# Kernel tuning notes

Measured on AMD Instinct MI355X. Metric: run time of the kernel, lower is better.

The kernel has to match this reference:

```python
import jax, jax.numpy as jnp
import numpy as np

N, HIDDEN, HEADS, HEAD = 20000, 128, 8, 16
LAP, NBUCKETS, NBINS, MAXDEG, E = 16, 1024, 32, 64, 320000


def _mlp(x, W1, b1, W2, b2):
    return jax.nn.relu(x @ W1 + b1) @ W2 + b2


def _build_pairs(bq, bk, edge_index):
    """Host-side: P_LSH = {(i,j)!=: bq[i]==bk[j]} union graph edges, deduped.
    Mirrors _lsh_pairs + torch.unique (data-dependent size -> numpy)."""
    bq = np.asarray(bq); bk = np.asarray(bk); ei = np.asarray(edge_index)
    srcs = [ei[0].astype(np.int64)]; dsts = [ei[1].astype(np.int64)]
    common = np.intersect1d(np.unique(bq), np.unique(bk))
    for b in common:
        qn = np.nonzero(bq == b)[0]
        kn = np.nonzero(bk == b)[0]
        ii = np.repeat(qn, kn.size)
        jj = np.tile(kn, qn.size)
        m = ii != jj
        srcs.append(ii[m].astype(np.int64)); dsts.append(jj[m].astype(np.int64))
    src = np.concatenate(srcs); dst = np.concatenate(dsts)
    code = np.unique(src * np.int64(N) + dst)  # dedup pairs
    return jnp.asarray(code // N, jnp.int32), jnp.asarray(code % N, jnp.int32)


def setup_inputs() -> dict:
    key = jax.random.key(0)
    ks = jax.random.split(key, 16)
    rn = lambda k, sh, s=1.0: (jax.random.normal(k, sh, jnp.float32) * s)
    d_in = HIDDEN + LAP
    return {
        "Q": rn(ks[0], (N, HIDDEN)),
        "K": rn(ks[1], (N, HIDDEN)),
        "V": rn(ks[2], (N, HIDDEN)),
        "lap_pe": jax.random.uniform(ks[3], (N, LAP), jnp.float32),
        "W_q1": rn(ks[4], (d_in, HIDDEN), d_in ** -0.5), "b_q1": jnp.zeros((HIDDEN,), jnp.float32),
        "W_q2": rn(ks[5], (HIDDEN, NBUCKETS), HIDDEN ** -0.5), "b_q2": jnp.zeros((NBUCKETS,), jnp.float32),
        "W_k1": rn(ks[6], (d_in, HIDDEN), d_in ** -0.5), "b_k1": jnp.zeros((HIDDEN,), jnp.float32),
        "W_k2": rn(ks[7], (HIDDEN, NBUCKETS), HIDDEN ** -0.5), "b_k2": jnp.zeros((NBUCKETS,), jnp.float32),
        "spd_bias": rn(ks[8], (NBINS + 1, HEADS), 0.02),
        "deg_src_emb": rn(ks[9], (MAXDEG + 2, HEADS), 0.02),
        "deg_dst_emb": rn(ks[10], (MAXDEG + 2, HEADS), 0.02),
        "W_out": rn(ks[11], (HIDDEN, HIDDEN), HIDDEN ** -0.5), "b_out": jnp.zeros((HIDDEN,), jnp.float32),
        "spd_boundaries": jnp.linspace(0.0, 2.0, NBINS).astype(jnp.float32),
        "edge_index": jax.random.randint(ks[12], (2, E), 0, N, jnp.int32),
        "deg": jax.random.randint(ks[13], (N,), 0, MAXDEG + 1, jnp.int32),
    }


def reference(Q, K, V, lap_pe, W_q1, b_q1, W_q2, b_q2, W_k1, b_k1, W_k2, b_k2,
              spd_bias, deg_src_emb, deg_dst_emb, W_out, b_out, spd_boundaries,
              edge_index, deg):
    q_in = jnp.concatenate([Q, lap_pe], axis=-1)
    k_in = jnp.concatenate([K, lap_pe], axis=-1)
    l_q = _mlp(q_in, W_q1, b_q1, W_q2, b_q2)  # (N, B)
    l_k = _mlp(k_in, W_k1, b_k1, W_k2, b_k2)
    src, dst = _build_pairs(jnp.argmax(l_q, -1), jnp.argmax(l_k, -1), edge_index)

    Qh = Q.reshape(N, HEADS, HEAD)
    Kh = K.reshape(N, HEADS, HEAD)
    Vh = V.reshape(N, HEADS, HEAD)

    scores = jnp.einsum("ehd,ehd->eh", Qh[src], Kh[dst]) / (HEAD ** 0.5)  # (P, H)
    pe_dist = jnp.linalg.norm(lap_pe[src] - lap_pe[dst], axis=-1)
    spd_idx = jnp.searchsorted(spd_boundaries, pe_dist, side="left")  # torch.bucketize(right=False)
    scores = scores + spd_bias[spd_idx]
    dsrc = jnp.clip(deg[src], 0, MAXDEG + 1)
    ddst = jnp.clip(deg[dst], 0, MAXDEG + 1)
    scores = scores + deg_src_emb[dsrc] + deg_dst_emb[ddst]

    # pyg_softmax: segment softmax over src index
    m = jax.ops.segment_max(scores, src, num_segments=N)  # (N, H)
    m = jnp.where(jnp.isneginf(m), 0.0, m)
    ex = jnp.exp(scores - m[src])
    denom = jax.ops.segment_sum(ex, src, num_segments=N)
    alpha = ex / (denom[src] + 1e-16)  # dropout p=0 (eval)

    h = jax.ops.segment_sum(alpha[..., None] * Vh[dst], src, num_segments=N)
    h_global = h.reshape(N, HIDDEN) @ W_out + b_out
    return h_global, l_q, l_k
```

## Files before the change

kernel.cpp:

```cpp
#include <hip/hip_runtime.h>
#include <math.h>

#define NN 20000
#define HID 128
#define NH 8
#define HD 16
#define LAPD 16
#define NB 1024
#define NBINS 32
#define MAXDEG 64
#define NE 320000
#define DIN 144

#define NEGH (-1.0e30f)

__global__ __launch_bounds__(256) void mlp_kernel(
    const float* __restrict__ X, const float* __restrict__ lap,
    const float* __restrict__ W1, const float* __restrict__ b1,
    const float* __restrict__ W2, const float* __restrict__ b2,
    float* __restrict__ outL, int* __restrict__ bidx)
{
    __shared__ __align__(16) float xs[16][DIN];
    __shared__ __align__(16) float hs[16][HID];
    __shared__ float rbv[64];
    __shared__ int   rbi[64];
    const int tid = threadIdx.x;
    const int n0 = blockIdx.x * 16;

    for (int e = tid; e < 16 * DIN; e += 256) {
        int n = e / DIN, k = e - n * DIN;
        float v = (k < HID) ? X[(size_t)(n0 + n) * HID + k]
                            : lap[(size_t)(n0 + n) * LAPD + (k - HID)];
        xs[n][k] = v;
    }
    __syncthreads();

    const int c = tid & 127, ng = tid >> 7;
    float hacc[8];
    {
        float bb = b1[c];
        #pragma unroll
        for (int m = 0; m < 8; m++) hacc[m] = bb;
        for (int k = 0; k < DIN; k += 4) {
            float w0 = W1[(k + 0) * HID + c];
            float w1 = W1[(k + 1) * HID + c];
            float w2 = W1[(k + 2) * HID + c];
            float w3 = W1[(k + 3) * HID + c];
            #pragma unroll
            for (int m = 0; m < 8; m++) {
                float4 xv = *(const float4*)&xs[ng * 8 + m][k];
                hacc[m] = fmaf(xv.x, w0, hacc[m]);
                hacc[m] = fmaf(xv.y, w1, hacc[m]);
                hacc[m] = fmaf(xv.z, w2, hacc[m]);
                hacc[m] = fmaf(xv.w, w3, hacc[m]);
            }
        }
    }
    #pragma unroll
    for (int m = 0; m < 8; m++) hs[ng * 8 + m][c] = fmaxf(hacc[m], 0.0f);
    __syncthreads();

    float a0[16], a1[16], a2[16], a3[16];
    #pragma unroll
    for (int m = 0; m < 16; m++) { a0[m] = 0.f; a1[m] = 0.f; a2[m] = 0.f; a3[m] = 0.f; }

    const float* W2b = W2 + 4 * tid;
    float4 w0 = *(const float4*)&W2b[(size_t)0 * NB];
    float4 w1 = *(const float4*)&W2b[(size_t)1 * NB];
    float4 w2 = *(const float4*)&W2b[(size_t)2 * NB];
    float4 w3 = *(const float4*)&W2b[(size_t)3 * NB];
    for (int k = 0; k < HID; k += 4) {
        const int kn = (k + 4 < HID) ? (k + 4) : 0;
        float4 nw0 = *(const float4*)&W2b[(size_t)(kn + 0) * NB];
        float4 nw1 = *(const float4*)&W2b[(size_t)(kn + 1) * NB];
        float4 nw2 = *(const float4*)&W2b[(size_t)(kn + 2) * NB];
        float4 nw3 = *(const float4*)&W2b[(size_t)(kn + 3) * NB];
        #pragma unroll
        for (int m = 0; m < 16; m++) {
            const float4 hv = *(const float4*)&hs[m][k];
            a0[m] = fmaf(hv.x, w0.x, fmaf(hv.y, w1.x, fmaf(hv.z, w2.x, fmaf(hv.w, w3.x, a0[m]))));
            a1[m] = fmaf(hv.x, w0.y, fmaf(hv.y, w1.y, fmaf(hv.z, w2.y, fmaf(hv.w, w3.y, a1[m]))));
            a2[m] = fmaf(hv.x, w0.z, fmaf(hv.y, w1.z, fmaf(hv.z, w2.z, fmaf(hv.w, w3.z, a2[m]))));
            a3[m] = fmaf(hv.x, w0.w, fmaf(hv.y, w1.w, fmaf(hv.z, w2.w, fmaf(hv.w, w3.w, a3[m]))));
        }
        w0 = nw0; w1 = nw1; w2 = nw2; w3 = nw3;
    }

    const float4 bb4 = *(const float4*)&b2[4 * tid];
    const int lane = tid & 63, wv = tid >> 6;
    const int o0 = 4 * tid;
    for (int m = 0; m < 16; m++) {
        float4 ov;
        ov.x = a0[m] + bb4.x; ov.y = a1[m] + bb4.y;
        ov.z = a2[m] + bb4.z; ov.w = a3[m] + bb4.w;
        *(float4*)&outL[(size_t)(n0 + m) * NB + o0] = ov;
        float bv = ov.x; int bi = o0;
        if (ov.y > bv) { bv = ov.y; bi = o0 + 1; }
        if (ov.z > bv) { bv = ov.z; bi = o0 + 2; }
        if (ov.w > bv) { bv = ov.w; bi = o0 + 3; }
        #pragma unroll
        for (int off = 1; off < 64; off <<= 1) {
            float ovv = __shfl_xor(bv, off, 64);
            int   oi  = __shfl_xor(bi, off, 64);
            if (ovv > bv || (ovv == bv && oi < bi)) { bv = ovv; bi = oi; }
        }
        if (lane == 0) { rbv[wv * 16 + m] = bv; rbi[wv * 16 + m] = bi; }
    }
    __syncthreads();
    if (tid < 16) {
        float bv = rbv[tid]; int bi = rbi[tid];
        #pragma unroll
        for (int ww = 1; ww < 4; ww++) {
            float ov = rbv[ww * 16 + tid]; int oi = rbi[ww * 16 + tid];
            if (ov > bv || (ov == bv && oi < bi)) { bv = ov; bi = oi; }
        }
        bidx[n0 + tid] = min(max(bi, 0), NB - 1);
    }
}

__global__ void zero_kernel(int* __restrict__ p, int n) {
    int i = blockIdx.x * 256 + threadIdx.x;
    if (i < n) p[i] = 0;
}

__global__ void hist_kernel(const int* __restrict__ bkarr, int* __restrict__ bcnt) {
    int i = blockIdx.x * 256 + threadIdx.x;
    if (i < NN) {
        int b = min(max(bkarr[i], 0), NB - 1);
        atomicAdd(&bcnt[b], 1);
    }
}

__global__ __launch_bounds__(1024) void scan_bucket_kernel(const int* __restrict__ cnt,
        int* __restrict__ off, int* __restrict__ fill) {
    __shared__ int s[1024];
    int t = threadIdx.x;
    int v = cnt[t];
    s[t] = v; __syncthreads();
    for (int o = 1; o < 1024; o <<= 1) {
        int a = (t >= o) ? s[t - o] : 0;
        __syncthreads();
        s[t] += a;
        __syncthreads();
    }
    int excl = s[t] - v;
    off[t] = excl; fill[t] = excl;
    if (t == 1023) off[NB] = s[1023];
}

__global__ __launch_bounds__(1024) void order_kernel(
    const int* __restrict__ boff,
    const int* __restrict__ qcnt,
    int* __restrict__ qfill)
{
    __shared__ int kk[1024];
    __shared__ int ii[1024];
    __shared__ int ss[1024];
    const int t = threadIdx.x;
    kk[t] = boff[t + 1] - boff[t];
    ii[t] = t;
    __syncthreads();
    for (int size = 2; size <= 1024; size <<= 1) {
        for (int stride = size >> 1; stride > 0; stride >>= 1) {
            const int p = t ^ stride;
            if (p > t) {
                const int k1 = kk[t], k2 = kk[p];
                const bool up = ((t & size) == 0);
                if ((k1 < k2) == up) {
                    const int i1 = ii[t];
                    kk[t] = k2; kk[p] = k1;
                    ii[t] = ii[p]; ii[p] = i1;
                }
            }
            __syncthreads();
        }
    }
    const int v = qcnt[ii[t]];
    ss[t] = v; __syncthreads();
    for (int o = 1; o < 1024; o <<= 1) {
        int a = (t >= o) ? ss[t - o] : 0;
        __syncthreads();
        ss[t] += a;
        __syncthreads();
    }
    qfill[ii[t]] = ss[t] - v;
}

__global__ void scatter_bucket_kernel(const int* __restrict__ bkarr,
        int* __restrict__ fill, int* __restrict__ blist) {
    int i = blockIdx.x * 256 + threadIdx.x;
    if (i < NN) {
        int b = min(max(bkarr[i], 0), NB - 1);
        int p = atomicAdd(&fill[b], 1);
        if (p >= 0 && p < NN) blist[p] = i;
    }
}

__global__ __launch_bounds__(1024) void scan_edge_kernel(const int* __restrict__ cnt,
        int* __restrict__ off, int* __restrict__ fill) {
    __shared__ int s[1024];
    const int t = threadIdx.x;
    const int base = t * 20;
    int loc[20]; int sum = 0;
    #pragma unroll
    for (int k = 0; k < 20; k++) {
        int idx = base + k;
        int v = (idx < NN) ? cnt[idx] : 0;
        loc[k] = sum; sum += v;
    }
    s[t] = sum; __syncthreads();
    for (int o = 1; o < 1024; o <<= 1) {
        int a = (t >= o) ? s[t - o] : 0;
        __syncthreads();
        s[t] += a;
        __syncthreads();
    }
    int pre = s[t] - sum;
    #pragma unroll
    for (int k = 0; k < 20; k++) {
        int idx = base + k;
        if (idx < NN) { int e = pre + loc[k]; off[idx] = e; fill[idx] = e; }
    }
    if (t == 1023) off[NN] = s[1023];
}

__global__ void edge_count_kernel(const int* __restrict__ ei, int* __restrict__ ecnt) {
    int e = blockIdx.x * 256 + threadIdx.x;
    if (e < NE) {
        int s = min(max(ei[e], 0), NN - 1);
        atomicAdd(&ecnt[s], 1);
    }
}

__global__ void edge_scatter_kernel(const int* __restrict__ ei,
        int* __restrict__ fill, int* __restrict__ adj) {
    int e = blockIdx.x * 256 + threadIdx.x;
    if (e < NE) {
        int s = min(max(ei[e], 0), NN - 1);
        int d = min(max(ei[NE + e], 0), NN - 1);
        int p = atomicAdd(&fill[s], 1);
        if (p >= 0 && p < NE) adj[p] = d;
    }
}

__global__ __launch_bounds__(256) void dedup_kernel(
    const int* __restrict__ eoff, int* __restrict__ adj,
    const int* __restrict__ bqv, const int* __restrict__ bkv,
    int* __restrict__ acnt)
{
    __shared__ int prev[4][192];
    const int lane = threadIdx.x & 63, wv = threadIdx.x >> 6;
    const int i = blockIdx.x * 4 + wv;
    if (i >= NN) return;
    int es = eoff[i], ee = eoff[i + 1];
    es = min(max(es, 0), NE); ee = min(max(ee, es), NE);
    const int d = ee - es;
    const int b = min(max(bqv[i], 0), NB - 1);
    int kept = 0;
    for (int t0 = 0; t0 < d; t0 += 64) {
        const int t = t0 + lane;
        const bool in = t < d;
        int j = -1;
        if (in) j = min(max(adj[es + t], 0), NN - 1);
        bool keep = in && ((j == i) || (bkv[j] != b));
        const int nin = min(64, d - t0);
        for (int q2 = 0; q2 < nin; q2++) {
            int jq = __shfl(j, q2, 64);
            if (in && q2 < lane && jq == j) keep = false;
        }
        if (t0 > 0 && in) {
            asm volatile("s_waitcnt lgkmcnt(0)" ::: "memory");
            const int np = min(t0, 192);
            for (int q2 = 0; q2 < np; q2++)
                if (prev[wv][q2] == j) keep = false;
        }
        if (in && t < 192) prev[wv][t] = j;
        unsigned long long km = __ballot(keep);
        int pos = __popcll(km & ((1ull << lane) - 1ull));
        if (keep) adj[es + kept + pos] = j;
        kept += (int)__popcll(km);
    }
    if (lane == 0) acnt[i] = kept;
}

__global__ __launch_bounds__(256) void attn_kernel(
    const float* __restrict__ Q, const float* __restrict__ K, const float* __restrict__ V,
    const float* __restrict__ lap,
    const float* __restrict__ spdb, const float* __restrict__ dse,
    const float* __restrict__ dde, const float* __restrict__ bndr,
    const int* __restrict__ deg,
    const int* __restrict__ bq,
    const int* __restrict__ boff, const int* __restrict__ blist,
    const int* __restrict__ eoff, const int* __restrict__ acnt,
    const int* __restrict__ adj, const int* __restrict__ qlist,
    float* __restrict__ outH)
{
    __shared__ __align__(16) float qfl[4][128];
    __shared__ __align__(16) float pefl[4][16];
    __shared__ float wts[4][8][66];
    __shared__ int   jls[4][64];
    __shared__ __align__(16) float spdbs[(NBINS + 1) * NH];
    __shared__ __align__(16) float ddes[(MAXDEG + 2) * NH];
    __shared__ float bnd[32];

    const int tid = threadIdx.x;
    const int wv = tid >> 6, lane = tid & 63;
    const int cq = lane >> 2, qq = lane & 3;

    const int task = (int)blockIdx.x * 4 + wv;
    int i = qlist[task];
    i = min(max(i, 0), NN - 1);

    for (int e = tid; e < (NBINS + 1) * NH; e += 256) spdbs[e] = spdb[e];
    for (int e = tid; e < (MAXDEG + 2) * NH; e += 256) ddes[e] = dde[e];
    if (tid < 32) bnd[tid] = bndr[tid];
    qfl[wv][lane]      = Q[(size_t)i * HID + lane];
    qfl[wv][lane + 64] = Q[(size_t)i * HID + 64 + lane];
    if (lane < 16) pefl[wv][lane] = lap[(size_t)i * LAPD + lane];

    int b = min(max(bq[i], 0), NB - 1);
    int bs = boff[b], be = boff[b + 1];
    bs = min(max(bs, 0), NN); be = min(max(be, bs), NN);
    int es = eoff[i];
    es = min(max(es, 0), NE);
    int na = min(max(acnt[i], 0), NE - es);
    const int Lb = be - bs;
    const int Ltot = Lb + na;
    const int degi = min(max(deg[i], 0), MAXDEG + 1);

    int jn = i; bool vn = false;
    if (lane < Ltot) {
        if (lane < Lb) {
            jn = min(max(blist[bs + lane], 0), NN - 1);
            vn = (jn != i);
        } else {
            jn = min(max(adj[es + (lane - Lb)], 0), NN - 1);
            vn = true;
        }
    }
    __syncthreads();

    const float4 ds0 = *(const float4*)&dse[degi * 8];
    const float4 ds1 = *(const float4*)&dse[degi * 8 + 4];

    float m8[8], l8[8];
    #pragma unroll
    for (int h = 0; h < 8; h++) { m8[h] = NEGH; l8[h] = 0.0f; }
    float acc[32];
    #pragma unroll
    for (int k = 0; k < 32; k++) acc[k] = 0.0f;

    for (int t0 = 0; t0 < Ltot; t0 += 64) {
        const int j = jn; const bool valid = vn;

        float s8[8];
        if (valid) {
            const float4* K4 = (const float4*)(K + (size_t)j * HID);
            const float4* Q4 = (const float4*)&qfl[wv][0];
            #pragma unroll
            for (int h = 0; h < 8; h++) {
                float4 k0 = K4[h * 4 + 0], k1 = K4[h * 4 + 1];
                float4 k2 = K4[h * 4 + 2], k3 = K4[h * 4 + 3];
                float4 q0 = Q4[h * 4 + 0], q1 = Q4[h * 4 + 1];
                float4 q2 = Q4[h * 4 + 2], q3 = Q4[h * 4 + 3];
                float dot = 0.0f;
                dot = fmaf(q0.x, k0.x, dot); dot = fmaf(q0.y, k0.y, dot);
                dot = fmaf(q0.z, k0.z, dot); dot = fmaf(q0.w, k0.w, dot);
                dot = fmaf(q1.x, k1.x, dot); dot = fmaf(q1.y, k1.y, dot);
                dot = fmaf(q1.z, k1.z, dot); dot = fmaf(q1.w, k1.w, dot);
                dot = fmaf(q2.x, k2.x, dot); dot = fmaf(q2.y, k2.y, dot);
                dot = fmaf(q2.z, k2.z, dot); dot = fmaf(q2.w, k2.w, dot);
                dot = fmaf(q3.x, k3.x, dot); dot = fmaf(q3.y, k3.y, dot);
                dot = fmaf(q3.z, k3.z, dot); dot = fmaf(q3.w, k3.w, dot);
                s8[h] = dot * 0.25f;
            }
            const float4* P4 = (const float4*)&pefl[wv][0];
            const float4* L4 = (const float4*)(lap + (size_t)j * LAPD);
            float ss = 0.0f;
            #pragma unroll
            for (int d4 = 0; d4 < 4; d4++) {
                float4 pe = P4[d4], lj = L4[d4];
                float dx = pe.x - lj.x, dy = pe.y - lj.y;
                float dz = pe.z - lj.z, dw = pe.w - lj.w;
                ss = fmaf(dx, dx, ss); ss = fmaf(dy, dy, ss);
                ss = fmaf(dz, dz, ss); ss = fmaf(dw, dw, ss);
            }
            float dist = sqrtf(ss);
            int si = 0;
            #pragma unroll
            for (int kb = 0; kb < 32; kb++) si += (bnd[kb] < dist) ? 1 : 0;
            const int dj = min(max(deg[j], 0), MAXDEG + 1);
            const float4 sb0 = *(const float4*)&spdbs[si * 8];
            const float4 sb1 = *(const float4*)&spdbs[si * 8 + 4];
            const float4 db0 = *(const float4*)&ddes[dj * 8];
            const float4 db1 = *(const float4*)&ddes[dj * 8 + 4];
            s8[0] += sb0.x + ds0.x + db0.x; s8[1] += sb0.y + ds0.y + db0.y;
            s8[2] += sb0.z + ds0.z + db0.z; s8[3] += sb0.w + ds0.w + db0.w;
            s8[4] += sb1.x + ds1.x + db1.x; s8[5] += sb1.y + ds1.y + db1.y;
            s8[6] += sb1.z + ds1.z + db1.z; s8[7] += sb1.w + ds1.w + db1.w;
        } else {
            #pragma unroll
            for (int h = 0; h < 8; h++) s8[h] = NEGH;
        }
        jls[wv][lane] = valid ? j : i;

        jn = i; vn = false;
        {
            const int t2 = t0 + 64 + lane;
            if (t2 < Ltot) {
                if (t2 < Lb) {
                    jn = min(max(blist[bs + t2], 0), NN - 1);
                    vn = (jn != i);
                } else {
                    jn = min(max(adj[es + (t2 - Lb)], 0), NN - 1);
                    vn = true;
                }
            }
        }

        float alpha8[8];
        #pragma unroll
        for (int h = 0; h < 8; h++) {
            float cm = s8[h];
            #pragma unroll
            for (int off = 1; off < 64; off <<= 1)
                cm = fmaxf(cm, __shfl_xor(cm, off, 64));
            const float mn = fmaxf(m8[h], cm);
            alpha8[h] = __expf(m8[h] - mn);
            const float p = valid ? __expf(s8[h] - mn) : 0.0f;
            l8[h] = l8[h] * alpha8[h] + p;
            m8[h] = mn;
            wts[wv][h][lane] = p;
        }

        float aq0, aq1;
        if (qq == 0)      { aq0 = alpha8[0]; aq1 = alpha8[1]; }
        else if (qq == 1) { aq0 = alpha8[2]; aq1 = alpha8[3]; }
        else if (qq == 2) { aq0 = alpha8[4]; aq1 = alpha8[5]; }
        else              { aq0 = alpha8[6]; aq1 = alpha8[7]; }

        #pragma unroll
        for (int k = 0; k < 16; k++) acc[k] *= aq0;
        #pragma unroll
        for (int k = 16; k < 32; k++) acc[k] *= aq1;

        asm volatile("s_waitcnt lgkmcnt(0)" ::: "memory");

        const int rem = Ltot - t0;
        const int npass = ((rem < 64 ? rem : 64) + 15) >> 4;
        for (int r = 0; r < npass; r++) {
            const int cc = r * 16 + cq;
            const int jc = jls[wv][cc];
            const float w0 = wts[wv][2 * qq][cc];
            const float w1 = wts[wv][2 * qq + 1][cc];
            const float4* V4 = (const float4*)(V + (size_t)jc * HID + qq * 32);
            #pragma unroll
            for (int s = 0; s < 4; s++) {
                const float4 v = V4[s];
                acc[s * 4 + 0] = fmaf(w0, v.x, acc[s * 4 + 0]);
                acc[s * 4 + 1] = fmaf(w0, v.y, acc[s * 4 + 1]);
                acc[s * 4 + 2] = fmaf(w0, v.z, acc[s * 4 + 2]);
                acc[s * 4 + 3] = fmaf(w0, v.w, acc[s * 4 + 3]);
            }
            #pragma unroll
            for (int s = 4; s < 8; s++) {
                const float4 v = V4[s];
                acc[s * 4 + 0] = fmaf(w1, v.x, acc[s * 4 + 0]);
                acc[s * 4 + 1] = fmaf(w1, v.y, acc[s * 4 + 1]);
                acc[s * 4 + 2] = fmaf(w1, v.z, acc[s * 4 + 2]);
                acc[s * 4 + 3] = fmaf(w1, v.w, acc[s * 4 + 3]);
            }
        }
    }

    #pragma unroll
    for (int h = 0; h < 8; h++) {
        float v = l8[h];
        #pragma unroll
        for (int off = 1; off < 64; off <<= 1) v += __shfl_xor(v, off, 64);
        l8[h] = v;
    }
    float lq0, lq1;
    if (qq == 0)      { lq0 = l8[0]; lq1 = l8[1]; }
    else if (qq == 1) { lq0 = l8[2]; lq1 = l8[3]; }
    else if (qq == 2) { lq0 = l8[4]; lq1 = l8[5]; }
    else              { lq0 = l8[6]; lq1 = l8[7]; }
    const float linv0 = 1.0f / (lq0 + 1e-16f);
    const float linv1 = 1.0f / (lq1 + 1e-16f);
    #pragma unroll
    for (int k = 0; k < 16; k++) acc[k] *= linv0;
    #pragma unroll
    for (int k = 16; k < 32; k++) acc[k] *= linv1;

    #pragma unroll
    for (int k = 0; k < 32; k++) {
        float v = acc[k];
        v += __shfl_xor(v, 4, 64);
        v += __shfl_xor(v, 8, 64);
        v += __shfl_xor(v, 16, 64);
        v += __shfl_xor(v, 32, 64);
        acc[k] = v;
    }
    if (cq == 0) {
        float4* orow = (float4*)(outH + (size_t)i * HID + qq * 32);
        #pragma unroll
        for (int s = 0; s < 8; s++)
            orow[s] = make_float4(acc[s * 4 + 0], acc[s * 4 + 1],
                                  acc[s * 4 + 2], acc[s * 4 + 3]);
    }
}

__global__ __launch_bounds__(256) void out_gemm_kernel(
    const float* __restrict__ Wout, const float* __restrict__ bout,
    float* __restrict__ outH)
{
    __shared__ __align__(16) float hsT[32][HID];
    const int tid = threadIdx.x;
    const int r0 = blockIdx.x * 32;

    for (int e = tid; e < 32 * 32; e += 256) {
        const int r = e >> 5, c4 = e & 31;
        ((float4*)&hsT[r][0])[c4] = ((const float4*)&outH[(size_t)(r0 + r) * HID])[c4];
    }
    __syncthreads();

    const int c = tid & 127;
    const int mg = tid >> 7;
    float acc[16];
    const float bb = bout[c];
    #pragma unroll
    for (int m = 0; m < 16; m++) acc[m] = bb;

    for (int k = 0; k < HID; k += 4) {
        const float w0 = Wout[(size_t)(k + 0) * HID + c];
        const float w1 = Wout[(size_t)(k + 1) * HID + c];
        const float w2 = Wout[(size_t)(k + 2) * HID + c];
        const float w3 = Wout[(size_t)(k + 3) * HID + c];
        #pragma unroll
        for (int m = 0; m < 16; m++) {
            const float4 hv = *(const float4*)&hsT[mg * 16 + m][k];
            acc[m] = fmaf(hv.x, w0, fmaf(hv.y, w1, fmaf(hv.z, w2, fmaf(hv.w, w3, acc[m]))));
        }
    }
    #pragma unroll
    for (int m = 0; m < 16; m++)
        outH[(size_t)(r0 + mg * 16 + m) * HID + c] = acc[m];
}

extern "C" void kernel_launch(void* const* d_in, const int* in_sizes, int n_in,
                              void* d_out, int out_size, void* d_ws, size_t ws_size,
                              hipStream_t stream) {
    const float* Q    = (const float*)d_in[0];
    const float* Kx   = (const float*)d_in[1];
    const float* Vx   = (const float*)d_in[2];
    const float* lap  = (const float*)d_in[3];
    const float* Wq1  = (const float*)d_in[4];
    const float* bq1  = (const float*)d_in[5];
    const float* Wq2  = (const float*)d_in[6];
    const float* bq2  = (const float*)d_in[7];
    const float* Wk1  = (const float*)d_in[8];
    const float* bk1  = (const float*)d_in[9];
    const float* Wk2  = (const float*)d_in[10];
    const float* bk2  = (const float*)d_in[11];
    const float* spdb = (const float*)d_in[12];
    const float* dse  = (const float*)d_in[13];
    const float* dde  = (const float*)d_in[14];
    const float* Wout = (const float*)d_in[15];
    const float* bout = (const float*)d_in[16];
    const float* bndr = (const float*)d_in[17];
    const int*   ei   = (const int*)d_in[18];
    const int*   deg  = (const int*)d_in[19];

    float* out   = (float*)d_out;
    float* outH  = out;
    float* outLq = out + (size_t)NN * HID;
    float* outLk = outLq + (size_t)NN * NB;

    int* wsp = (int*)d_ws;
    size_t o = 0;
    auto carve = [&](size_t n_ints) -> int* {
        int* p = wsp + o; o += n_ints; return p;
    };
    int* bcnt  = carve(NB);
    int* boff  = carve(NB + 1);
    int* bfill = carve(NB);
    int* blist = carve(NN);
    int* bqv   = carve(NN);
    int* bkv   = carve(NN);
    int* ecnt  = carve(NN);
    int* eoff  = carve(NN + 1);
    int* efill = carve(NN);
    int* adj   = carve(NE);
    int* qlist = carve(NN);

    zero_kernel<<<(NB + 255) / 256, 256, 0, stream>>>(bcnt, NB);
    zero_kernel<<<(NN + 255) / 256, 256, 0, stream>>>(ecnt, NN);

    mlp_kernel<<<NN / 16, 256, 0, stream>>>(Q,  lap, Wq1, bq1, Wq2, bq2, outLq, bqv);
    mlp_kernel<<<NN / 16, 256, 0, stream>>>(Kx, lap, Wk1, bk1, Wk2, bk2, outLk, bkv);

    hist_kernel<<<(NN + 255) / 256, 256, 0, stream>>>(bkv, bcnt);
    scan_bucket_kernel<<<1, 1024, 0, stream>>>(bcnt, boff, bfill);
    scatter_bucket_kernel<<<(NN + 255) / 256, 256, 0, stream>>>(bkv, bfill, blist);

    zero_kernel<<<(NB + 255) / 256, 256, 0, stream>>>(bcnt, NB);
    hist_kernel<<<(NN + 255) / 256, 256, 0, stream>>>(bqv, bcnt);
    order_kernel<<<1, 1024, 0, stream>>>(boff, bcnt, bfill);
    scatter_bucket_kernel<<<(NN + 255) / 256, 256, 0, stream>>>(bqv, bfill, qlist);

    edge_count_kernel<<<(NE + 255) / 256, 256, 0, stream>>>(ei, ecnt);
    scan_edge_kernel<<<1, 1024, 0, stream>>>(ecnt, eoff, efill);
    edge_scatter_kernel<<<(NE + 255) / 256, 256, 0, stream>>>(ei, efill, adj);

    dedup_kernel<<<NN / 4, 256, 0, stream>>>(eoff, adj, bqv, bkv, ecnt);

    attn_kernel<<<NN / 4, 256, 0, stream>>>(Q, Kx, Vx, lap, spdb, dse, dde, bndr, deg,
                                            bqv, boff, blist, eoff, ecnt, adj, qlist,
                                            outH);

    out_gemm_kernel<<<NN / 32, 256, 0, stream>>>(Wout, bout, outH);
}
```

Before: 832.2 us.

## Split long-row attention nodes across eight waves with partial softmax merge

Adds a partition kernel that separates nodes whose candidate list (bucket size plus adjacency count) exceeds a threshold. Each such node gets a whole 512-thread block whose eight waves process disjoint segments, then merge their online-softmax states through shared memory. Small nodes are packed eight per block as before. This targets load imbalance, where a few nodes in large LSH buckets leave one wave running long. The cost is an extra single-block kernel, a grid of NN blocks where most exit early, and larger blocks that may lower occupancy.

```diff
diff --git a/kernel.cpp b/kernel.cpp
--- a/kernel.cpp
+++ b/kernel.cpp
@@ -11,6 +11,8 @@
 #define MAXDEG 64
 #define NE 320000
 #define DIN 144
+#define NW 8
+#define THRESH 512
 
 #define NEGH (-1.0e30f)
 
@@ -283,7 +285,50 @@
     if (lane == 0) acnt[i] = kept;
 }
 
-__global__ __launch_bounds__(256) void attn_kernel(
+__global__ __launch_bounds__(1024) void partition_kernel(
+    const int* __restrict__ qlist, const int* __restrict__ bqv,
+    const int* __restrict__ boff, const int* __restrict__ acnt,
+    int* __restrict__ biglist, int* __restrict__ smalllist, int* __restrict__ cnts)
+{
+    __shared__ int s[1024];
+    const int t = threadIdx.x;
+    const int base = t * 20;
+    int loc[20], nid[20], flg[20];
+    int sum = 0;
+    #pragma unroll
+    for (int k = 0; k < 20; k++) {
+        const int p = base + k;
+        int big = 0, n = 0;
+        if (p < NN) {
+            n = min(max(qlist[p], 0), NN - 1);
+            const int b = min(max(bqv[n], 0), NB - 1);
+            const int L = (boff[b + 1] - boff[b]) + min(max(acnt[n], 0), NE);
+            big = (L > THRESH) ? 1 : 0;
+        }
+        nid[k] = n; flg[k] = big;
+        loc[k] = sum; sum += big;
+    }
+    s[t] = sum; __syncthreads();
+    for (int o = 1; o < 1024; o <<= 1) {
+        int a = (t >= o) ? s[t - o] : 0;
+        __syncthreads();
+        s[t] += a;
+        __syncthreads();
+    }
+    const int pre = s[t] - sum;
+    #pragma unroll
+    for (int k = 0; k < 20; k++) {
+        const int p = base + k;
+        if (p < NN) {
+            const int bb = pre + loc[k];
+            if (flg[k]) biglist[bb] = nid[k];
+            else        smalllist[p - bb] = nid[k];
+        }
+    }
+    if (t == 1023) cnts[0] = s[1023];
+}
+
+__global__ __launch_bounds__(512) void attn_kernel(
     const float* __restrict__ Q, const float* __restrict__ K, const float* __restrict__ V,
     const float* __restrict__ lap,
     const float* __restrict__ spdb, const float* __restrict__ dse,
@@ -292,27 +337,46 @@
     const int* __restrict__ bq,
     const int* __restrict__ boff, const int* __restrict__ blist,
     const int* __restrict__ eoff, const int* __restrict__ acnt,
-    const int* __restrict__ adj, const int* __restrict__ qlist,
+    const int* __restrict__ adj,
+    const int* __restrict__ biglist, const int* __restrict__ smalllist,
+    const int* __restrict__ cnts,
     float* __restrict__ outH)
 {
-    __shared__ __align__(16) float qfl[4][128];
-    __shared__ __align__(16) float pefl[4][16];
-    __shared__ float wts[4][8][66];
-    __shared__ int   jls[4][64];
+    __shared__ __align__(16) float qfl[NW][128];
+    __shared__ __align__(16) float pefl[NW][16];
+    __shared__ float wts[NW][8][66];
+    __shared__ int   jls[NW][64];
     __shared__ __align__(16) float spdbs[(NBINS + 1) * NH];
     __shared__ __align__(16) float ddes[(MAXDEG + 2) * NH];
     __shared__ float bnd[32];
+    __shared__ float mrgm[NW][8], mrgl[NW][8];
+    __shared__ float hpart[NW][128];
+    __shared__ float ltot_s[8];
 
     const int tid = threadIdx.x;
     const int wv = tid >> 6, lane = tid & 63;
     const int cq = lane >> 2, qq = lane & 3;
 
-    const int task = (int)blockIdx.x * 4 + wv;
-    int i = qlist[task];
+    int nbig = min(max(cnts[0], 0), NN);
+    const int nsmall = NN - nbig;
+    const int nblocks = nbig + (nsmall + NW - 1) / NW;
+    const int br = (int)blockIdx.x;
+    if (br >= nblocks) return;
+
+    const bool bigm = (br < nbig);
+    bool active = true;
+    int i;
+    if (bigm) {
+        i = biglist[br];
+    } else {
+        const int task = (br - nbig) * NW + wv;
+        active = (task < nsmall);
+        i = active ? smalllist[task] : 0;
+    }
     i = min(max(i, 0), NN - 1);
 
-    for (int e = tid; e < (NBINS + 1) * NH; e += 256) spdbs[e] = spdb[e];
-    for (int e = tid; e < (MAXDEG + 2) * NH; e += 256) ddes[e] = dde[e];
+    for (int e = tid; e < (NBINS + 1) * NH; e += 512) spdbs[e] = spdb[e];
+    for (int e = tid; e < (MAXDEG + 2) * NH; e += 512) ddes[e] = dde[e];
     if (tid < 32) bnd[tid] = bndr[tid];
     qfl[wv][lane]      = Q[(size_t)i * HID + lane];
     qfl[wv][lane + 64] = Q[(size_t)i * HID + 64 + lane];
@@ -328,14 +392,25 @@
     const int Ltot = Lb + na;
     const int degi = min(max(deg[i], 0), MAXDEG + 1);
 
+    int tb = 0, te = Ltot;
+    if (bigm) {
+        const int Lseg = (Ltot + NW - 1) / NW;
+        tb = min(wv * Lseg, Ltot);
+        te = min(tb + Lseg, Ltot);
+    }
+    if (!active) { tb = 0; te = 0; }
+
     int jn = i; bool vn = false;
-    if (lane < Ltot) {
-        if (lane < Lb) {
-            jn = min(max(blist[bs + lane], 0), NN - 1);
-            vn = (jn != i);
-        } else {
-            jn = min(max(adj[es + (lane - Lb)], 0), NN - 1);
-            vn = true;
+    {
+        const int t = tb + lane;
+        if (t < te) {
+            if (t < Lb) {
+                jn = min(max(blist[bs + t], 0), NN - 1);
+                vn = (jn != i);
+            } else {
+                jn = min(max(adj[es + (t - Lb)], 0), NN - 1);
+                vn = true;
+            }
         }
     }
     __syncthreads();
@@ -350,7 +425,7 @@
     #pragma unroll
     for (int k = 0; k < 32; k++) acc[k] = 0.0f;
 
-    for (int t0 = 0; t0 < Ltot; t0 += 64) {
+    for (int t0 = tb; t0 < te; t0 += 64) {
         const int j = jn; const bool valid = vn;
 
         float s8[8];
@@ -407,7 +482,7 @@
         jn = i; vn = false;
         {
             const int t2 = t0 + 64 + lane;
-            if (t2 < Ltot) {
+            if (t2 < te) {
                 if (t2 < Lb) {
                     jn = min(max(blist[bs + t2], 0), NN - 1);
                     vn = (jn != i);
@@ -446,7 +521,7 @@
 
         asm volatile("s_waitcnt lgkmcnt(0)" ::: "memory");
 
-        const int rem = Ltot - t0;
+        const int rem = te - t0;
         const int npass = ((rem < 64 ? rem : 64) + 15) >> 4;
         for (int r = 0; r < npass; r++) {
             const int cc = r * 16 + cq;
@@ -480,33 +555,87 @@
         for (int off = 1; off < 64; off <<= 1) v += __shfl_xor(v, off, 64);
         l8[h] = v;
     }
-    float lq0, lq1;
-    if (qq == 0)      { lq0 = l8[0]; lq1 = l8[1]; }
-    else if (qq == 1) { lq0 = l8[2]; lq1 = l8[3]; }
-    else if (qq == 2) { lq0 = l8[4]; lq1 = l8[5]; }
-    else              { lq0 = l8[6]; lq1 = l8[7]; }
-    const float linv0 = 1.0f / (lq0 + 1e-16f);
-    const float linv1 = 1.0f / (lq1 + 1e-16f);
-    #pragma unroll
-    for (int k = 0; k < 16; k++) acc[k] *= linv0;
-    #pragma unroll
-    for (int k = 16; k < 32; k++) acc[k] *= linv1;
-
-    #pragma unroll
-    for (int k = 0; k < 32; k++) {
-        float v = acc[k];
-        v += __shfl_xor(v, 4, 64);
-        v += __shfl_xor(v, 8, 64);
-        v += __shfl_xor(v, 16, 64);
-        v += __shfl_xor(v, 32, 64);
-        acc[k] = v;
-    }
-    if (cq == 0) {
-        float4* orow = (float4*)(outH + (size_t)i * HID + qq * 32);
-        #pragma unroll
-        for (int s = 0; s < 8; s++)
-            orow[s] = make_float4(acc[s * 4 + 0], acc[s * 4 + 1],
-                                  acc[s * 4 + 2], acc[s * 4 + 3]);
+
+    if (bigm) {
+        if (lane == 0) {
+            #pragma unroll
+            for (int h = 0; h < 8; h++) { mrgm[wv][h] = m8[h]; mrgl[wv][h] = l8[h]; }
+        }
+        __syncthreads();
+        float ma_, mb_;
+        if (qq == 0)      { ma_ = m8[0]; mb_ = m8[1]; }
+        else if (qq == 1) { ma_ = m8[2]; mb_ = m8[3]; }
+        else if (qq == 2) { ma_ = m8[4]; mb_ = m8[5]; }
+        else              { ma_ = m8[6]; mb_ = m8[7]; }
+        float Ma = mrgm[0][2 * qq], Mb = mrgm[0][2 * qq + 1];
+        #pragma unroll
+        for (int w = 1; w < NW; w++) {
+            Ma = fmaxf(Ma, mrgm[w][2 * qq]);
+            Mb = fmaxf(Mb, mrgm[w][2 * qq + 1]);
+        }
+        const float fa = __expf(ma_ - Ma);
+        const float fb = __expf(mb_ - Mb);
+        #pragma unroll
+        for (int k = 0; k < 16; k++) acc[k] *= fa;
+        #pragma unroll
+        for (int k = 16; k < 32; k++) acc[k] *= fb;
+        #pragma unroll
+        for (int k = 0; k < 32; k++) {
+            float v = acc[k];
+            v += __shfl_xor(v, 4, 64);
+            v += __shfl_xor(v, 8, 64);
+            v += __shfl_xor(v, 16, 64);
+            v += __shfl_xor(v, 32, 64);
+            acc[k] = v;
+        }
+        if (cq == 0) {
+            #pragma unroll
+            for (int k = 0; k < 32; k++) hpart[wv][qq * 32 + k] = acc[k];
+        }
+        if (tid < 8) {
+            float M = mrgm[0][tid];
+            #pragma unroll
+            for (int w = 1; w < NW; w++) M = fmaxf(M, mrgm[w][tid]);
+            float lt = 0.0f;
+            #pragma unroll
+            for (int w = 0; w < NW; w++) lt += mrgl[w][tid] * __expf(mrgm[w][tid] - M);
+            ltot_s[tid] = lt;
+        }
+        __syncthreads();
+        if (tid < 128) {
+            float sum = hpart[0][tid];
+            #pragma unroll
+            for (int w = 1; w < NW; w++) sum += hpart[w][tid];
+            outH[(size_t)i * HID + tid] = sum / (ltot_s[tid >> 4] + 1e-16f);
+        }
+    } else {
+        float lq0, lq1;
+        if (qq == 0)      { lq0 = l8[0]; lq1 = l8[1]; }
+        else if (qq == 1) { lq0 = l8[2]; lq1 = l8[3]; }
+        else if (qq == 2) { lq0 = l8[4]; lq1 = l8[5]; }
+        else              { lq0 = l8[6]; lq1 = l8[7]; }
+        const float linv0 = 1.0f / (lq0 + 1e-16f);
+        const float linv1 = 1.0f / (lq1 + 1e-16f);
+        #pragma unroll
+        for (int k = 0; k < 16; k++) acc[k] *= linv0;
+        #pragma unroll
+        for (int k = 16; k < 32; k++) acc[k] *= linv1;
+        #pragma unroll
+        for (int k = 0; k < 32; k++) {
+            float v = acc[k];
+            v += __shfl_xor(v, 4, 64);
+            v += __shfl_xor(v, 8, 64);
+            v += __shfl_xor(v, 16, 64);
+            v += __shfl_xor(v, 32, 64);
+            acc[k] = v;
+        }
+        if (active && cq == 0) {
+            float4* orow = (float4*)(outH + (size_t)i * HID + qq * 32);
+            #pragma unroll
+            for (int s = 0; s < 8; s++)
+                orow[s] = make_float4(acc[s * 4 + 0], acc[s * 4 + 1],
+                                      acc[s * 4 + 2], acc[s * 4 + 3]);
+        }
     }
 }
 
@@ -581,17 +710,20 @@
     auto carve = [&](size_t n_ints) -> int* {
         int* p = wsp + o; o += n_ints; return p;
     };
-    int* bcnt  = carve(NB);
-    int* boff  = carve(NB + 1);
-    int* bfill = carve(NB);
-    int* blist = carve(NN);
-    int* bqv   = carve(NN);
-    int* bkv   = carve(NN);
-    int* ecnt  = carve(NN);
-    int* eoff  = carve(NN + 1);
-    int* efill = carve(NN);
-    int* adj   = carve(NE);
-    int* qlist = carve(NN);
+    int* bcnt   = carve(NB);
+    int* boff   = carve(NB + 1);
+    int* bfill  = carve(NB);
+    int* blist  = carve(NN);
+    int* bqv    = carve(NN);
+    int* bkv    = carve(NN);
+    int* ecnt   = carve(NN);
+    int* eoff   = carve(NN + 1);
+    int* efill  = carve(NN);
+    int* adj    = carve(NE);
+    int* qlist  = carve(NN);
+    int* biglist   = carve(NN);
+    int* smalllist = carve(NN);
+    int* cnts   = carve(4);
 
     zero_kernel<<<(NB + 255) / 256, 256, 0, stream>>>(bcnt, NB);
     zero_kernel<<<(NN + 255) / 256, 256, 0, stream>>>(ecnt, NN);
@@ -614,9 +746,12 @@
 
     dedup_kernel<<<NN / 4, 256, 0, stream>>>(eoff, adj, bqv, bkv, ecnt);
 
-    attn_kernel<<<NN / 4, 256, 0, stream>>>(Q, Kx, Vx, lap, spdb, dse, dde, bndr, deg,
-                                            bqv, boff, blist, eoff, ecnt, adj, qlist,
-                                            outH);
+    partition_kernel<<<1, 1024, 0, stream>>>(qlist, bqv, boff, ecnt,
+                                             biglist, smalllist, cnts);
+
+    attn_kernel<<<NN, 512, 0, stream>>>(Q, Kx, Vx, lap, spdb, dse, dde, bndr, deg,
+                                        bqv, boff, blist, eoff, ecnt, adj,
+                                        biglist, smalllist, cnts, outH);
 
     out_gemm_kernel<<<NN / 32, 256, 0, stream>>>(Wout, bout, outH);
 }
```

New measurement: 823.2 us. Within noise of the previous version (-1.1%).
